# Performance work log

Hardware: AMD Instinct MI355X
Metric: run time of the kernel (lower is better)

Reference implementation:

```python
import jax, jax.numpy as jnp
import numpy as np

TEMP = 0.1
EPS = 1e-8  # torch cosine_similarity eps
B, P, N, D = 256, 32, 512, 256


def setup_inputs() -> dict:
    key = jax.random.key(0)
    k1, k2, k3 = jax.random.split(key, 3)
    return {
        "anchors": jax.random.normal(k1, (B, D), dtype=jnp.float32),
        "positives": jax.random.normal(k2, (B, P, D), dtype=jnp.float32),
        "negatives": jax.random.normal(k3, (B, N, D), dtype=jnp.float32),
    }


def reference(anchors, positives, negatives):
    # all_samples: (B, K, D) with K = P + N
    all_samples = jnp.concatenate([positives, negatives], axis=1)
    # Cosine similarity of anchor vs every sample (the original broadcasts the
    # anchor over P identical rows; we compute the (B, K) row once).
    dots = jnp.einsum("bd,bkd->bk", anchors, all_samples)          # (B, K)
    na = jnp.linalg.norm(anchors, axis=-1, keepdims=True)           # (B, 1)
    nk = jnp.linalg.norm(all_samples, axis=-1)                      # (B, K)
    sim = dots / jnp.maximum(na * nk, EPS) / TEMP                   # (B, K)
    logp = jax.nn.log_softmax(sim, axis=-1)                         # (B, K)
    p = positives.shape[1]
    # labels = arange(P): gather picks -log_softmax at column p for row p;
    # since all P rows equal, this is just the first P columns of logp.
    return -jnp.mean(logp[:, :p])
```

## Files before the change

### kernel.cpp

```cpp
#include <hip/hip_runtime.h>
#include <math.h>

#define TEMP_INV 10.0f
#define EPS 1e-8f
#define B_ 256
#define P_ 32
#define N_ 512
#define D_ 256
#define K_ (P_ + N_)
#define G_ (K_ / 4)

__device__ __forceinline__ float wave_reduce_sum(float v) {
    #pragma unroll
    for (int m = 32; m >= 1; m >>= 1) v += __shfl_xor(v, m, 64);
    return v;
}

__device__ __forceinline__ float wave_reduce_max(float v) {
    #pragma unroll
    for (int m = 32; m >= 1; m >>= 1) v = fmaxf(v, __shfl_xor(v, m, 64));
    return v;
}

__device__ __forceinline__ float dot4(float4 a, float4 b) {
    return a.x * b.x + a.y * b.y + a.z * b.z + a.w * b.w;
}

__global__ __launch_bounds__(256) void sim_kernel(
    const float* __restrict__ anchors,
    const float* __restrict__ positives,
    const float* __restrict__ negatives,
    float* __restrict__ sim,
    float* __restrict__ out) {
    int gw   = blockIdx.x * 4 + (threadIdx.x >> 6);
    int lane = threadIdx.x & 63;
    int b  = gw / G_;
    int g  = gw - b * G_;
    int k0 = g * 4;

    const float4* a4 = (const float4*)(anchors + (size_t)b * D_);
    float4 a = a4[lane];

    const float4* base = (k0 < P_)
        ? (const float4*)(positives + ((size_t)b * P_ + k0) * D_)
        : (const float4*)(negatives + ((size_t)b * N_ + (k0 - P_)) * D_);

    float4 s0 = base[lane];
    float4 s1 = base[64 + lane];
    float4 s2 = base[128 + lane];
    float4 s3 = base[192 + lane];

    float na = sqrtf(wave_reduce_sum(dot4(a, a)));

    float d0 = wave_reduce_sum(dot4(a, s0));
    float q0 = wave_reduce_sum(dot4(s0, s0));
    float d1 = wave_reduce_sum(dot4(a, s1));
    float q1 = wave_reduce_sum(dot4(s1, s1));
    float d2 = wave_reduce_sum(dot4(a, s2));
    float q2 = wave_reduce_sum(dot4(s2, s2));
    float d3 = wave_reduce_sum(dot4(a, s3));
    float q3 = wave_reduce_sum(dot4(s3, s3));

    if (lane == 0) {
        float* row = sim + (size_t)b * K_ + k0;
        row[0] = d0 / fmaxf(na * sqrtf(q0), EPS) * TEMP_INV;
        row[1] = d1 / fmaxf(na * sqrtf(q1), EPS) * TEMP_INV;
        row[2] = d2 / fmaxf(na * sqrtf(q2), EPS) * TEMP_INV;
        row[3] = d3 / fmaxf(na * sqrtf(q3), EPS) * TEMP_INV;
    }

    if (blockIdx.x == 0 && threadIdx.x == 0) out[0] = 0.0f;
}

__global__ __launch_bounds__(256) void softmax_kernel(
    const float* __restrict__ sim,
    float* __restrict__ out) {
    int b    = blockIdx.x;
    int tid  = threadIdx.x;
    int wid  = tid >> 6;
    int lane = tid & 63;
    const float* row = sim + (size_t)b * K_;

    float vals[3];
    int cnt = 0;
    float lmax = -INFINITY;
    for (int k = tid; k < K_; k += 256) {
        float v = row[k];
        vals[cnt++] = v;
        lmax = fmaxf(lmax, v);
    }

    __shared__ float s_max[4];
    __shared__ float s_sum[4];
    __shared__ float s_pos[4];

    float wmax = wave_reduce_max(lmax);
    if (lane == 0) s_max[wid] = wmax;
    __syncthreads();
    float bmax = fmaxf(fmaxf(s_max[0], s_max[1]), fmaxf(s_max[2], s_max[3]));

    float lsum = 0.0f;
    for (int i = 0; i < cnt; i++) lsum += expf(vals[i] - bmax);
    float wsum = wave_reduce_sum(lsum);
    if (lane == 0) s_sum[wid] = wsum;

    float lp = (tid < P_) ? vals[0] : 0.0f;
    float wp = wave_reduce_sum(lp);
    if (lane == 0) s_pos[wid] = wp;
    __syncthreads();

    if (tid == 0) {
        float bsum = s_sum[0] + s_sum[1] + s_sum[2] + s_sum[3];
        float bpos = s_pos[0] + s_pos[1] + s_pos[2] + s_pos[3];
        float lse  = bmax + logf(bsum);
        float partial = ((float)P_ * lse - bpos) * (1.0f / (float)(B_ * P_));
        atomicAdd(out, partial);
    }
}

extern "C" void kernel_launch(void* const* d_in, const int* in_sizes, int n_in,
                              void* d_out, int out_size, void* d_ws, size_t ws_size,
                              hipStream_t stream) {
    const float* anchors   = (const float*)d_in[0];
    const float* positives = (const float*)d_in[1];
    const float* negatives = (const float*)d_in[2];
    float* out = (float*)d_out;
    float* sim = (float*)d_ws;

    int n_waves  = B_ * G_;
    int n_blocks = n_waves / 4;
    sim_kernel<<<n_blocks, 256, 0, stream>>>(anchors, positives, negatives, sim, out);
    softmax_kernel<<<B_, 256, 0, stream>>>(sim, out);
}
```

Measured before the change: 202.1 us.

## Fuse similarity and log-softmax into one kernel with one block per batch row

Replaces the two-kernel pipeline with a single kernel that gives each batch row one 1024-thread block. Its 16 waves compute the cosine similarities two rows at a time into shared memory, then the block does the max/sum-exp/positive reduction and an atomic add. This removes the global intermediate sim buffer, its write and re-read, and the second kernel launch. The trade-off is only 256 blocks, one per batch row, with a serial unroll-1 loop of two loads per iteration. That may cut memory-level parallelism on a bandwidth-bound workload, and the output is now zeroed by an extra memset call.

```diff
diff --git a/kernel.cpp b/kernel.cpp
--- a/kernel.cpp
+++ b/kernel.cpp
@@ -8,7 +8,8 @@
 #define N_ 512
 #define D_ 256
 #define K_ (P_ + N_)
-#define G_ (K_ / 4)
+#define NWAVE 16
+#define ROWS_PER_WAVE (K_ / NWAVE)
 
 __device__ __forceinline__ float wave_reduce_sum(float v) {
     #pragma unroll
@@ -26,93 +27,73 @@
     return a.x * b.x + a.y * b.y + a.z * b.z + a.w * b.w;
 }
 
-__global__ __launch_bounds__(256) void sim_kernel(
+__global__ __launch_bounds__(1024) void fused_kernel(
     const float* __restrict__ anchors,
     const float* __restrict__ positives,
     const float* __restrict__ negatives,
-    float* __restrict__ sim,
-    float* __restrict__ out) {
-    int gw   = blockIdx.x * 4 + (threadIdx.x >> 6);
-    int lane = threadIdx.x & 63;
-    int b  = gw / G_;
-    int g  = gw - b * G_;
-    int k0 = g * 4;
-
-    const float4* a4 = (const float4*)(anchors + (size_t)b * D_);
-    float4 a = a4[lane];
-
-    const float4* base = (k0 < P_)
-        ? (const float4*)(positives + ((size_t)b * P_ + k0) * D_)
-        : (const float4*)(negatives + ((size_t)b * N_ + (k0 - P_)) * D_);
-
-    float4 s0 = base[lane];
-    float4 s1 = base[64 + lane];
-    float4 s2 = base[128 + lane];
-    float4 s3 = base[192 + lane];
-
-    float na = sqrtf(wave_reduce_sum(dot4(a, a)));
-
-    float d0 = wave_reduce_sum(dot4(a, s0));
-    float q0 = wave_reduce_sum(dot4(s0, s0));
-    float d1 = wave_reduce_sum(dot4(a, s1));
-    float q1 = wave_reduce_sum(dot4(s1, s1));
-    float d2 = wave_reduce_sum(dot4(a, s2));
-    float q2 = wave_reduce_sum(dot4(s2, s2));
-    float d3 = wave_reduce_sum(dot4(a, s3));
-    float q3 = wave_reduce_sum(dot4(s3, s3));
-
-    if (lane == 0) {
-        float* row = sim + (size_t)b * K_ + k0;
-        row[0] = d0 / fmaxf(na * sqrtf(q0), EPS) * TEMP_INV;
-        row[1] = d1 / fmaxf(na * sqrtf(q1), EPS) * TEMP_INV;
-        row[2] = d2 / fmaxf(na * sqrtf(q2), EPS) * TEMP_INV;
-        row[3] = d3 / fmaxf(na * sqrtf(q3), EPS) * TEMP_INV;
-    }
-
-    if (blockIdx.x == 0 && threadIdx.x == 0) out[0] = 0.0f;
-}
-
-__global__ __launch_bounds__(256) void softmax_kernel(
-    const float* __restrict__ sim,
     float* __restrict__ out) {
     int b    = blockIdx.x;
     int tid  = threadIdx.x;
     int wid  = tid >> 6;
     int lane = tid & 63;
-    const float* row = sim + (size_t)b * K_;
 
-    float vals[3];
-    int cnt = 0;
-    float lmax = -INFINITY;
-    for (int k = tid; k < K_; k += 256) {
-        float v = row[k];
-        vals[cnt++] = v;
-        lmax = fmaxf(lmax, v);
+    __shared__ float s_sim[K_];
+    __shared__ float s_red[3 * NWAVE];
+
+    const float4* a4 = (const float4*)(anchors + (size_t)b * D_);
+    float4 a = a4[lane];
+    float na = sqrtf(wave_reduce_sum(dot4(a, a)));
+
+    const float4* pos4 = (const float4*)(positives + (size_t)b * P_ * D_);
+    const float4* neg4 = (const float4*)(negatives + (size_t)b * N_ * D_);
+
+    #pragma unroll 1
+    for (int i = 0; i < ROWS_PER_WAVE; i += 2) {
+        int k0 = wid * ROWS_PER_WAVE + i;
+        int k1 = k0 + 1;
+        const float4* p0 = (k0 < P_) ? (pos4 + (size_t)k0 * 64)
+                                     : (neg4 + (size_t)(k0 - P_) * 64);
+        const float4* p1 = (k1 < P_) ? (pos4 + (size_t)k1 * 64)
+                                     : (neg4 + (size_t)(k1 - P_) * 64);
+        float4 s0 = p0[lane];
+        float4 s1 = p1[lane];
+        float d0 = wave_reduce_sum(dot4(a, s0));
+        float q0 = wave_reduce_sum(dot4(s0, s0));
+        float d1 = wave_reduce_sum(dot4(a, s1));
+        float q1 = wave_reduce_sum(dot4(s1, s1));
+        if (lane == 0) {
+            s_sim[k0] = d0 / fmaxf(na * sqrtf(q0), EPS) * TEMP_INV;
+            s_sim[k1] = d1 / fmaxf(na * sqrtf(q1), EPS) * TEMP_INV;
+        }
     }
+    __syncthreads();
 
-    __shared__ float s_max[4];
-    __shared__ float s_sum[4];
-    __shared__ float s_pos[4];
+    float v = (tid < K_) ? s_sim[tid] : -INFINITY;
+    float wmax = wave_reduce_max(v);
+    if (lane == 0) s_red[wid] = wmax;
+    __syncthreads();
+    float bmax = s_red[0];
+    #pragma unroll
+    for (int j = 1; j < NWAVE; j++) bmax = fmaxf(bmax, s_red[j]);
 
-    float wmax = wave_reduce_max(lmax);
-    if (lane == 0) s_max[wid] = wmax;
-    __syncthreads();
-    float bmax = fmaxf(fmaxf(s_max[0], s_max[1]), fmaxf(s_max[2], s_max[3]));
-
-    float lsum = 0.0f;
-    for (int i = 0; i < cnt; i++) lsum += expf(vals[i] - bmax);
-    float wsum = wave_reduce_sum(lsum);
-    if (lane == 0) s_sum[wid] = wsum;
-
-    float lp = (tid < P_) ? vals[0] : 0.0f;
+    float e  = (tid < K_) ? expf(v - bmax) : 0.0f;
+    float ws = wave_reduce_sum(e);
+    float lp = (tid < P_) ? v : 0.0f;
     float wp = wave_reduce_sum(lp);
-    if (lane == 0) s_pos[wid] = wp;
+    if (lane == 0) {
+        s_red[NWAVE + wid]     = ws;
+        s_red[2 * NWAVE + wid] = wp;
+    }
     __syncthreads();
 
     if (tid == 0) {
-        float bsum = s_sum[0] + s_sum[1] + s_sum[2] + s_sum[3];
-        float bpos = s_pos[0] + s_pos[1] + s_pos[2] + s_pos[3];
-        float lse  = bmax + logf(bsum);
+        float bsum = 0.0f, bpos = 0.0f;
+        #pragma unroll
+        for (int j = 0; j < NWAVE; j++) {
+            bsum += s_red[NWAVE + j];
+            bpos += s_red[2 * NWAVE + j];
+        }
+        float lse = bmax + logf(bsum);
         float partial = ((float)P_ * lse - bpos) * (1.0f / (float)(B_ * P_));
         atomicAdd(out, partial);
     }
@@ -125,10 +106,7 @@
     const float* positives = (const float*)d_in[1];
     const float* negatives = (const float*)d_in[2];
     float* out = (float*)d_out;
-    float* sim = (float*)d_ws;
 
-    int n_waves  = B_ * G_;
-    int n_blocks = n_waves / 4;
-    sim_kernel<<<n_blocks, 256, 0, stream>>>(anchors, positives, negatives, sim, out);
-    softmax_kernel<<<B_, 256, 0, stream>>>(sim, out);
+    hipMemsetAsync(out, 0, sizeof(float), stream);
+    fused_kernel<<<B_, NWAVE * 64, 0, stream>>>(anchors, positives, negatives, out);
 }
```

New measurement: 208.1 us. 1.03x slower.
